# Kernel optimization log

Measured on AMD Instinct MI355X. Metric: run time of the kernel, lower is better.

The kernel has to match this reference:

```python
import jax, jax.numpy as jnp
import numpy as np

B, S, N, E, H = 256, 64, 64, 128, 128
CCLIP = 10.0
NEG = 1e8


def setup_inputs() -> dict:
    key = jax.random.key(0)
    ks = jax.random.split(key, 12)
    u = lambda k, shp, s=1.0: jax.random.uniform(k, shp, minval=-s, maxval=s)
    s = 1.0 / float(np.sqrt(E))
    return dict(
        node_context=jax.random.normal(ks[0], (B, S, N, E), jnp.float32),
        original_data=jax.random.normal(ks[1], (B, S, N, 2), jnp.float32),
        cell_context=jax.random.normal(ks[2], (B, S, E), jnp.float32),
        high_mask=jnp.zeros((B, S), jnp.int32),
        low_mask=jnp.zeros((B, S, N), jnp.int32),
        init_w=u(ks[3], (2 * E,)),
        h_W=u(ks[4], (E, E), s), h_b=jnp.zeros((E,), jnp.float32),
        vw_W=u(ks[5], (2 * E, E), s), vw_b=jnp.zeros((E,), jnp.float32),
        Wq=u(ks[6], (E, H), s), bq=jnp.zeros((H,), jnp.float32),
        Wk=u(ks[7], (E, H), s), bk=jnp.zeros((H,), jnp.float32),
        v=u(ks[8], (H,), s), vb=jnp.zeros((), jnp.float32),
        w_low=u(ks[9], (E,), s),
    )


def _decode(node_context, original_data, cell_context, high_mask, low_mask,
            init_w, h_W, h_b, vw_W, vw_b, Wq, bq, Wk, bk, v, vb, w_low):
    base = jax.random.key(42)
    bidx = jnp.arange(B)
    # query init: h_bar + v_weight_embed(init_w)
    h_bar = cell_context.mean(axis=1) @ h_W + h_b              # [B,E]
    query0 = h_bar + init_w @ vw_W + vw_b                      # [B,E]
    # pointer keys are fixed across steps (target = cell_context)
    keys = jnp.einsum('bse,eh->bsh', cell_context, Wk) + bk    # [B,S,H]

    def step(carry, i):
        query, mask, init_h, last_node = carry
        # Pointer: u = C * tanh(v . tanh(Wq q + Wk t)), masked softmax
        q = query @ Wq + bq                                    # [B,H]
        u_ = jnp.tanh(q[:, None, :] + keys) @ v + vb           # [B,S]
        u_ = CCLIP * jnp.tanh(u_) - NEG * mask.astype(u_.dtype)
        logp = jax.nn.log_softmax(u_, axis=-1)
        idx = jax.random.categorical(jax.random.fold_in(base, i), u_)
        idx = jnp.where(i == 0, jnp.zeros_like(idx), idx)      # forced start cell
        cell_lp = logp[bidx, idx]                              # [B]
        # batched per-cell gathers (replaces the torch per-batch python loop)
        cur_cell = node_context[bidx, idx]                     # [B,N,E]
        orig_cell = original_data[bidx, idx]                   # [B,N,2]
        cur_mask = low_mask[bidx, idx]                         # [B,N]
        # simplified low-level decoder surrogate (external module in torch)
        low_logits = cur_cell @ w_low - NEG * cur_mask.astype(cur_cell.dtype)
        low_lp = jax.nn.log_softmax(low_logits, axis=-1).sum(axis=-1)  # [B]
        low_act = jnp.argmax(low_logits, axis=-1)              # [B]
        i_n = orig_cell[:, 0, :]                               # entry node [B,2]
        l_n = orig_cell[:, -1, :]                              # exit node  [B,2]
        low_reward = jnp.sqrt((jnp.diff(orig_cell, axis=1) ** 2).sum(-1)).sum(-1)
        cell_reward = jnp.sqrt(((last_node - i_n) ** 2).sum(-1))  # [B]
        # Environment.update_state: mask out the visited cell
        mask = jnp.maximum(mask, jax.nn.one_hot(idx, S, dtype=mask.dtype))
        h = cell_context[bidx, idx]                            # [B,E]
        init_h = jnp.where(i == 0, h, init_h)
        query = h_bar + jnp.concatenate([init_h, h], axis=-1) @ vw_W + vw_b
        return (query, mask, init_h, l_n), (cell_lp, low_lp, cell_reward, low_reward, idx, low_act)

    carry0 = (query0, high_mask,
              jnp.zeros((B, E), query0.dtype), jnp.zeros((B, 2), query0.dtype))
    _, (hlp, llp, hr, lr, hact, lact) = jax.lax.scan(step, carry0, jnp.arange(S))
    return (hlp.sum(0), llp.sum(0), hr.sum(0), lr.sum(0), hact.T, lact.T)


def reference(node_context, original_data, cell_context, high_mask, low_mask,
              init_w, h_W, h_b, vw_W, vw_b, Wq, bq, Wk, bk, v, vb, w_low):
    return _decode(node_context, original_data, cell_context, high_mask, low_mask,
                   init_w, h_W, h_b, vw_W, vw_b, Wq, bq, Wk, bk, v, vb, w_low)
```

## Files before the change

### kernel.cpp

```cpp
#include <hip/hip_runtime.h>
#include <stdint.h>


#define NB 256
#define NS 64
#define NN 64
#define NE 128
#define NH 128
#define NEGC 1.0e8f

#define WS_KEYS 0
#define WS_P    (WS_KEYS + NB*NS*NH)
#define WS_C0   (WS_P + NB*NS*NH)
#define WS_Q0   (WS_C0 + NB*NH)
#define WS_U    (WS_Q0 + NB*NH)
#define WS_GUM  (WS_U + NB*65*64)
#define WS_LLP  (WS_GUM + NB*64*64)
#define WS_LRW  (WS_LLP + NB*NS)
#define WS_LAC  (WS_LRW + NB*NS)
#define WS_INX  (WS_LAC + NB*NS)
#define WS_LNX  (WS_INX + NB*NS*2)

__device__ __forceinline__ void tf2x32(uint32_t k0, uint32_t k1,
                                       uint32_t x0, uint32_t x1,
                                       uint32_t &o0, uint32_t &o1) {
  const uint32_t R[5][4] = {{13,15,26,6},{17,29,16,24},{13,15,26,6},{17,29,16,24},{13,15,26,6}};
  uint32_t ks[3] = {k0, k1, k0 ^ k1 ^ 0x1BD11BDAu};
  x0 += ks[0]; x1 += ks[1];
  #pragma unroll
  for (int g = 0; g < 5; ++g) {
    #pragma unroll
    for (int r = 0; r < 4; ++r) {
      x0 += x1;
      uint32_t d = R[g][r];
      x1 = (x1 << d) | (x1 >> (32 - d));
      x1 ^= x0;
    }
    x0 += ks[(g + 1) % 3];
    x1 += ks[(g + 2) % 3] + (uint32_t)(g + 1);
  }
  o0 = x0; o1 = x1;
}

__device__ __forceinline__ float gumbel_from(uint32_t fk0, uint32_t fk1, int e) {
  uint32_t a0, a1, x0, x1;
  if (e < 8192) { x0 = (uint32_t)e; x1 = (uint32_t)(e + 8192); }
  else          { x0 = (uint32_t)(e - 8192); x1 = (uint32_t)e; }
  tf2x32(fk0, fk1, x0, x1, a0, a1);
  uint32_t bits = (e < 8192) ? a0 : a1;
  uint32_t fb = (bits >> 9) | 0x3F800000u;
  float f = __uint_as_float(fb) - 1.0f;
  const float tiny = 1.17549435e-38f;
  float u = fmaxf(tiny, f + tiny);
  return (float)(-log(-log((double)u)));
}

__global__ __launch_bounds__(256) void k_main(
    const float* __restrict__ node,
    const float* __restrict__ orig,
    const float* __restrict__ cellc,
    const int*   __restrict__ lmask,
    const float* __restrict__ init_w,
    const float* __restrict__ hW,
    const float* __restrict__ hb,
    const float* __restrict__ vwW,
    const float* __restrict__ vwb,
    const float* __restrict__ Wq,
    const float* __restrict__ bq,
    const float* __restrict__ Wk,
    const float* __restrict__ bk,
    const float* __restrict__ wlow,
    float* __restrict__ ws)
{
  __shared__ float s_t[NS * 132];
  __shared__ float s_cm[NE], s_hbar[NE], s_base[NE], s_q0e[NE];
  const int t = threadIdx.x;
  const int blk = blockIdx.x;

  if (blk < NB) {
    const int b = blk;
    const float* cb = cellc + (size_t)b * NS * NE;
    const int g = t & 31, sg = t >> 5;
    const int hh0 = 4 * g;

    {
      float acc[8][4];
      #pragma unroll
      for (int r = 0; r < 8; ++r) { acc[r][0]=acc[r][1]=acc[r][2]=acc[r][3]=0.f; }
      for (int k = 0; k < NE; k += 4) {
        float4 w0 = *(const float4*)&Wk[(k+0)*NH+hh0];
        float4 w1 = *(const float4*)&Wk[(k+1)*NH+hh0];
        float4 w2 = *(const float4*)&Wk[(k+2)*NH+hh0];
        float4 w3 = *(const float4*)&Wk[(k+3)*NH+hh0];
        #pragma unroll
        for (int r = 0; r < 8; ++r) {
          float4 c4 = *(const float4*)&cb[(sg*8+r)*NE+k];
          acc[r][0] += c4.x*w0.x + c4.y*w1.x + c4.z*w2.x + c4.w*w3.x;
          acc[r][1] += c4.x*w0.y + c4.y*w1.y + c4.z*w2.y + c4.w*w3.y;
          acc[r][2] += c4.x*w0.z + c4.y*w1.z + c4.z*w2.z + c4.w*w3.z;
          acc[r][3] += c4.x*w0.w + c4.y*w1.w + c4.z*w2.w + c4.w*w3.w;
        }
      }
      float4 bb = *(const float4*)&bk[hh0];
      #pragma unroll
      for (int r = 0; r < 8; ++r) {
        float4 o = make_float4(acc[r][0]+bb.x, acc[r][1]+bb.y, acc[r][2]+bb.z, acc[r][3]+bb.w);
        *(float4*)&ws[WS_KEYS + (size_t)b*NS*NH + (sg*8+r)*NH + hh0] = o;
      }
    }
    {
      const float* Vb = vwW + NE * NE;
      float acc[8][4];
      #pragma unroll
      for (int r = 0; r < 8; ++r) { acc[r][0]=acc[r][1]=acc[r][2]=acc[r][3]=0.f; }
      for (int k = 0; k < NE; k += 4) {
        float4 w0 = *(const float4*)&Vb[(k+0)*NE+hh0];
        float4 w1 = *(const float4*)&Vb[(k+1)*NE+hh0];
        float4 w2 = *(const float4*)&Vb[(k+2)*NE+hh0];
        float4 w3 = *(const float4*)&Vb[(k+3)*NE+hh0];
        #pragma unroll
        for (int r = 0; r < 8; ++r) {
          float4 c4 = *(const float4*)&cb[(sg*8+r)*NE+k];
          acc[r][0] += c4.x*w0.x + c4.y*w1.x + c4.z*w2.x + c4.w*w3.x;
          acc[r][1] += c4.x*w0.y + c4.y*w1.y + c4.z*w2.y + c4.w*w3.y;
          acc[r][2] += c4.x*w0.z + c4.y*w1.z + c4.z*w2.z + c4.w*w3.z;
          acc[r][3] += c4.x*w0.w + c4.y*w1.w + c4.z*w2.w + c4.w*w3.w;
        }
      }
      #pragma unroll
      for (int r = 0; r < 8; ++r)
        *(float4*)&s_t[(sg*8+r)*132 + hh0] =
            make_float4(acc[r][0], acc[r][1], acc[r][2], acc[r][3]);
    }
    if (t < NE) {
      float a = 0.f;
      for (int s = 0; s < NS; ++s) a += cb[s*NE+t];
      s_cm[t] = a * (1.0f/64.0f);
    }
    __syncthreads();
    {
      float acc[8][4];
      #pragma unroll
      for (int r = 0; r < 8; ++r) { acc[r][0]=acc[r][1]=acc[r][2]=acc[r][3]=0.f; }
      for (int k = 0; k < NE; k += 4) {
        float4 w0 = *(const float4*)&Wq[(k+0)*NH+hh0];
        float4 w1 = *(const float4*)&Wq[(k+1)*NH+hh0];
        float4 w2 = *(const float4*)&Wq[(k+2)*NH+hh0];
        float4 w3 = *(const float4*)&Wq[(k+3)*NH+hh0];
        #pragma unroll
        for (int r = 0; r < 8; ++r) {
          float4 c4 = *(const float4*)&s_t[(sg*8+r)*132 + k];
          acc[r][0] += c4.x*w0.x + c4.y*w1.x + c4.z*w2.x + c4.w*w3.x;
          acc[r][1] += c4.x*w0.y + c4.y*w1.y + c4.z*w2.y + c4.w*w3.y;
          acc[r][2] += c4.x*w0.z + c4.y*w1.z + c4.z*w2.z + c4.w*w3.z;
          acc[r][3] += c4.x*w0.w + c4.y*w1.w + c4.z*w2.w + c4.w*w3.w;
        }
      }
      #pragma unroll
      for (int r = 0; r < 8; ++r)
        *(float4*)&ws[WS_P + (size_t)b*NS*NH + (sg*8+r)*NH + hh0] =
            make_float4(acc[r][0], acc[r][1], acc[r][2], acc[r][3]);
    }
    if (t < NE) {
      float a0=0,a1=0,a2=0,a3=0;
      for (int k = 0; k < NE; k += 4) {
        a0 += s_cm[k+0]*hW[(k+0)*NE+t]; a1 += s_cm[k+1]*hW[(k+1)*NE+t];
        a2 += s_cm[k+2]*hW[(k+2)*NE+t]; a3 += s_cm[k+3]*hW[(k+3)*NE+t];
      }
      s_hbar[t] = (a0+a1)+(a2+a3) + hb[t];
    }
    __syncthreads();
    if (t < NE) {
      float a0=0,a1=0,a2=0,a3=0;
      for (int k = 0; k < NE; k += 4) {
        a0 += cb[k+0]*vwW[(k+0)*NE+t]; a1 += cb[k+1]*vwW[(k+1)*NE+t];
        a2 += cb[k+2]*vwW[(k+2)*NE+t]; a3 += cb[k+3]*vwW[(k+3)*NE+t];
      }
      s_base[t] = s_hbar[t] + (a0+a1)+(a2+a3) + vwb[t];
      float e0=0,e1=0,e2=0,e3=0;
      for (int k = 0; k < 2*NE; k += 4) {
        e0 += init_w[k+0]*vwW[(k+0)*NE+t]; e1 += init_w[k+1]*vwW[(k+1)*NE+t];
        e2 += init_w[k+2]*vwW[(k+2)*NE+t]; e3 += init_w[k+3]*vwW[(k+3)*NE+t];
      }
      s_q0e[t] = s_hbar[t] + (e0+e1)+(e2+e3) + vwb[t];
    }
    __syncthreads();
    if (t < NH) {
      float a0=0,a1=0,a2=0,a3=0, b0=0,b1=0,b2=0,b3=0;
      for (int e = 0; e < NE; e += 4) {
        float w0=Wq[(e+0)*NH+t], w1=Wq[(e+1)*NH+t], w2=Wq[(e+2)*NH+t], w3=Wq[(e+3)*NH+t];
        a0 += s_base[e+0]*w0; a1 += s_base[e+1]*w1; a2 += s_base[e+2]*w2; a3 += s_base[e+3]*w3;
        b0 += s_q0e[e+0]*w0;  b1 += s_q0e[e+1]*w1;  b2 += s_q0e[e+2]*w2;  b3 += s_q0e[e+3]*w3;
      }
      ws[WS_C0 + b*NH + t] = (a0+a1)+(a2+a3) + bq[t];
      ws[WS_Q0 + b*NH + t] = (b0+b1)+(b2+b3) + bq[t];
    }
  } else if (blk < NB + 4096) {
    const int l = blk - NB;
    const int b = l >> 4;
    const int w = t >> 6, lane = t & 63;
    const int s = ((l & 15) << 2) + w;
    const size_t row = (size_t)(b*NS + s)*NN + lane;
    const float4* nr4 = (const float4*)(node + row * (size_t)NE);
    const float4* wl4 = (const float4*)wlow;
    float a0=0,a1=0,a2=0,a3=0;
    #pragma unroll 8
    for (int j = 0; j < 32; j += 4) {
      float4 n0=nr4[j], n1=nr4[j+1], n2=nr4[j+2], n3=nr4[j+3];
      float4 w0=wl4[j], w1=wl4[j+1], w2=wl4[j+2], w3=wl4[j+3];
      a0 += n0.x*w0.x + n0.y*w0.y + n0.z*w0.z + n0.w*w0.w;
      a1 += n1.x*w1.x + n1.y*w1.y + n1.z*w1.z + n1.w*w1.w;
      a2 += n2.x*w2.x + n2.y*w2.y + n2.z*w2.z + n2.w*w2.w;
      a3 += n3.x*w3.x + n3.y*w3.y + n3.z*w3.z + n3.w*w3.w;
    }
    float logit = (a0+a1)+(a2+a3) - NEGC * (float)lmask[row];
    float m2 = logit;
    #pragma unroll
    for (int off = 32; off; off >>= 1) m2 = fmaxf(m2, __shfl_xor(m2, off));
    float se = expf(logit - m2);
    float ss = logit;
    float bv = logit; int bi = lane;
    #pragma unroll
    for (int off = 32; off; off >>= 1) {
      se += __shfl_xor(se, off);
      ss += __shfl_xor(ss, off);
      float ov = __shfl_xor(bv, off); int oi = __shfl_xor(bi, off);
      if (ov > bv || (ov == bv && oi < bi)) { bv = ov; bi = oi; }
    }
    float2 og = ((const float2*)orig)[row];
    float nx = __shfl(og.x, (lane+1)&63), ny = __shfl(og.y, (lane+1)&63);
    float dd = 0.f;
    if (lane < 63) {
      float dx = nx - og.x, dy = ny - og.y;
      dd = sqrtf(dx*dx + dy*dy);
    }
    #pragma unroll
    for (int off = 32; off; off >>= 1) dd += __shfl_xor(dd, off);
    const int o = b*NS + s;
    if (lane == 0) {
      ws[WS_LLP + o] = ss - 64.f*(m2 + logf(se));
      ws[WS_LRW + o] = dd;
      ws[WS_LAC + o] = (float)bi;
      ws[WS_INX + 2*o]   = og.x;
      ws[WS_INX + 2*o+1] = og.y;
    }
    if (lane == 63) {
      ws[WS_LNX + 2*o]   = og.x;
      ws[WS_LNX + 2*o+1] = og.y;
    }
  } else {
    const int gblk = blk - NB - 4096;
    const int i = gblk >> 4;
    const int b = ((gblk & 15) << 4) + (t >> 4);
    const int s4 = (t & 15) << 2;
    uint32_t fk0, fk1;
    tf2x32(0u, 42u, 0u, (uint32_t)i, fk0, fk1);
    float4 o;
    o.x = gumbel_from(fk0, fk1, b*64 + s4 + 0);
    o.y = gumbel_from(fk0, fk1, b*64 + s4 + 1);
    o.z = gumbel_from(fk0, fk1, b*64 + s4 + 2);
    o.w = gumbel_from(fk0, fk1, b*64 + s4 + 3);
    *(float4*)&ws[WS_GUM + (size_t)b*4096 + i*64 + s4] = o;
  }
}

__global__ __launch_bounds__(256) void k_u(const float* __restrict__ vvec,
                                           const float* __restrict__ vb_p,
                                           float* __restrict__ ws)
{
  __shared__ float s_keys[NS * 129];
  __shared__ float s_q[4 * NE];
  __shared__ float s_v[NH];
  const int t = threadIdx.x;
  const int b = blockIdx.x >> 3, rb = blockIdx.x & 7;
  const int nrows = (rb == 7) ? 9 : 8;
  {
    const int s = t >> 2, h0 = (t & 3) * 32;
    const float* src = ws + WS_KEYS + (size_t)b*NS*NH + s*NH + h0;
    #pragma unroll
    for (int j = 0; j < 8; ++j) {
      float4 v4 = *(const float4*)&src[4*j];
      s_keys[s*129 + h0 + 4*j + 0] = v4.x;
      s_keys[s*129 + h0 + 4*j + 1] = v4.y;
      s_keys[s*129 + h0 + 4*j + 2] = v4.z;
      s_keys[s*129 + h0 + 4*j + 3] = v4.w;
    }
  }
  if (t < NH) s_v[t] = vvec[t];
  __syncthreads();
  const float vb = vb_p[0];
  const int w = t >> 6, lane = t & 63;
  for (int r = w; r < nrows; r += 4) {
    const int jj = rb*8 + r;
    {
      const float* c0p = ws + WS_C0 + b*NH;
      const float* q0p = ws + WS_Q0 + b*NH;
      const float* Pp  = ws + WS_P + (size_t)b*NS*NH + (size_t)jj*NH;
      float v1, v2;
      if (jj == 64) { v1 = q0p[lane]; v2 = q0p[lane+64]; }
      else          { v1 = c0p[lane] + Pp[lane]; v2 = c0p[lane+64] + Pp[lane+64]; }
      s_q[w*NE + lane]      = v1;
      s_q[w*NE + lane + 64] = v2;
    }
    float acc = 0.f;
    #pragma unroll 4
    for (int h = 0; h < NH; ++h) {
      float qk = s_q[w*NE + h] + s_keys[lane*129 + h];
      acc += tanhf(qk) * s_v[h];
    }
    ws[WS_U + (size_t)b*4160 + jj*64 + lane] = 10.f * tanhf(acc + vb);
  }
}

__global__ __launch_bounds__(64) void k_loop(const int* __restrict__ hmask,
                                             float* __restrict__ out,
                                             const float* __restrict__ ws)
{
  __shared__ float s_U[65 * 64];
  __shared__ float s_gum[64 * 64];
  const int lane = threadIdx.x;
  const int b = blockIdx.x;
  for (int j = lane; j < 65*64; j += 64) s_U[j] = ws[WS_U + (size_t)b*4160 + j];
  for (int j = lane; j < 64*64; j += 64) s_gum[j] = ws[WS_GUM + (size_t)b*4096 + j];
  const int o = b*NS + lane;
  const float lowlp  = ws[WS_LLP + o];
  const float lowrew = ws[WS_LRW + o];
  const float lowact = ws[WS_LAC + o];
  const float inx = ws[WS_INX + 2*o], iny = ws[WS_INX + 2*o+1];
  const float lnx = ws[WS_LNX + 2*o], lny = ws[WS_LNX + 2*o+1];
  float msk = (float)hmask[o];
  float hlp = 0.f, llp = 0.f, hr = 0.f, lr = 0.f;
  float pnx = 0.f, pny = 0.f;
  int prev = 64;
  for (int i = 0; i < NS; ++i) {
    float logit = s_U[prev*64 + lane] - NEGC * msk;
    float pert  = logit + s_gum[i*64 + lane];
    float m = logit, bv = pert; int bi = lane;
    #pragma unroll
    for (int off = 32; off; off >>= 1) {
      m = fmaxf(m, __shfl_xor(m, off));
      float ov = __shfl_xor(bv, off); int oi = __shfl_xor(bi, off);
      if (ov > bv || (ov == bv && oi < bi)) { bv = ov; bi = oi; }
    }
    float se = expf(logit - m);
    #pragma unroll
    for (int off = 32; off; off >>= 1) se += __shfl_xor(se, off);
    const int idx = (i == 0) ? 0 : bi;
    float li = __shfl(logit, idx);
    hlp += li - m - logf(se);
    llp += __shfl(lowlp, idx);
    lr  += __shfl(lowrew, idx);
    float ix = __shfl(inx, idx), iy = __shfl(iny, idx);
    float dx = pnx - ix, dy = pny - iy;
    hr += sqrtf(dx*dx + dy*dy);
    pnx = __shfl(lnx, idx); pny = __shfl(lny, idx);
    float lact_v = __shfl(lowact, idx);
    if (lane == 0) {
      out[4*NB + b*NS + i] = (float)idx;
      out[4*NB + NB*NS + b*NS + i] = lact_v;
    }
    if (lane == idx) msk = 1.f;
    prev = idx;
  }
  if (lane == 0) {
    out[b]        = hlp;
    out[NB + b]   = llp;
    out[2*NB + b] = hr;
    out[3*NB + b] = lr;
  }
}

extern "C" void kernel_launch(void* const* d_in, const int* in_sizes, int n_in,
                              void* d_out, int out_size, void* d_ws, size_t ws_size,
                              hipStream_t stream) {
  (void)in_sizes; (void)n_in; (void)out_size; (void)ws_size;
  const float* node   = (const float*)d_in[0];
  const float* orig   = (const float*)d_in[1];
  const float* cellc  = (const float*)d_in[2];
  const int*   hmask  = (const int*)d_in[3];
  const int*   lmask  = (const int*)d_in[4];
  const float* init_w = (const float*)d_in[5];
  const float* hW     = (const float*)d_in[6];
  const float* hb     = (const float*)d_in[7];
  const float* vwW    = (const float*)d_in[8];
  const float* vwb    = (const float*)d_in[9];
  const float* Wq     = (const float*)d_in[10];
  const float* bq     = (const float*)d_in[11];
  const float* Wk     = (const float*)d_in[12];
  const float* bk     = (const float*)d_in[13];
  const float* v      = (const float*)d_in[14];
  const float* vb     = (const float*)d_in[15];
  const float* wlow   = (const float*)d_in[16];
  float* ws  = (float*)d_ws;
  float* out = (float*)d_out;

  k_main<<<dim3(NB + 4096 + 1024), dim3(256), 0, stream>>>(
      node, orig, cellc, lmask, init_w, hW, hb, vwW, vwb,
      Wq, bq, Wk, bk, wlow, ws);
  k_u<<<dim3(2048), dim3(256), 0, stream>>>(v, vb, ws);
  k_loop<<<dim3(NB), dim3(64), 0, stream>>>(hmask, out, ws);
}
```

Before: 952.0 us.

## Interleave node-context streaming with pointer-logit compute in one fused kernel

The memory-bound low-level node scoring moves out of the prep kernel and into the pointer-logit kernel. Blocks are interleaved in a 2:1 pattern, so bandwidth-heavy streaming overlaps with tanh-heavy compute. The per-batch prep work is split across two blocks to expose more parallelism. Shared-memory key and U/Gumbel staging is vectorized with float4 and a padded stride. The cost is more complex block indexing and one half-block that repeats only part of the prep work.

```diff
diff --git a/kernel.cpp b/kernel.cpp
--- a/kernel.cpp
+++ b/kernel.cpp
@@ -55,11 +55,8 @@
   return (float)(-log(-log((double)u)));
 }
 
-__global__ __launch_bounds__(256) void k_main(
-    const float* __restrict__ node,
-    const float* __restrict__ orig,
+__global__ __launch_bounds__(256) void k_prep(
     const float* __restrict__ cellc,
-    const int*   __restrict__ lmask,
     const float* __restrict__ init_w,
     const float* __restrict__ hW,
     const float* __restrict__ hb,
@@ -69,32 +66,32 @@
     const float* __restrict__ bq,
     const float* __restrict__ Wk,
     const float* __restrict__ bk,
-    const float* __restrict__ wlow,
     float* __restrict__ ws)
 {
-  __shared__ float s_t[NS * 132];
+  __shared__ __align__(16) float s_t[32 * 132];
   __shared__ float s_cm[NE], s_hbar[NE], s_base[NE], s_q0e[NE];
   const int t = threadIdx.x;
   const int blk = blockIdx.x;
 
-  if (blk < NB) {
-    const int b = blk;
+  if (blk < 2 * NB) {
+    const int b = blk >> 1, half = blk & 1, s0 = half * 32;
     const float* cb = cellc + (size_t)b * NS * NE;
     const int g = t & 31, sg = t >> 5;
     const int hh0 = 4 * g;
+    const int r0 = s0 + sg * 4;
 
     {
-      float acc[8][4];
-      #pragma unroll
-      for (int r = 0; r < 8; ++r) { acc[r][0]=acc[r][1]=acc[r][2]=acc[r][3]=0.f; }
+      float acc[4][4];
+      #pragma unroll
+      for (int r = 0; r < 4; ++r) { acc[r][0]=acc[r][1]=acc[r][2]=acc[r][3]=0.f; }
       for (int k = 0; k < NE; k += 4) {
         float4 w0 = *(const float4*)&Wk[(k+0)*NH+hh0];
         float4 w1 = *(const float4*)&Wk[(k+1)*NH+hh0];
         float4 w2 = *(const float4*)&Wk[(k+2)*NH+hh0];
         float4 w3 = *(const float4*)&Wk[(k+3)*NH+hh0];
         #pragma unroll
-        for (int r = 0; r < 8; ++r) {
-          float4 c4 = *(const float4*)&cb[(sg*8+r)*NE+k];
+        for (int r = 0; r < 4; ++r) {
+          float4 c4 = *(const float4*)&cb[(r0+r)*NE+k];
           acc[r][0] += c4.x*w0.x + c4.y*w1.x + c4.z*w2.x + c4.w*w3.x;
           acc[r][1] += c4.x*w0.y + c4.y*w1.y + c4.z*w2.y + c4.w*w3.y;
           acc[r][2] += c4.x*w0.z + c4.y*w1.z + c4.z*w2.z + c4.w*w3.z;
@@ -103,24 +100,23 @@
       }
       float4 bb = *(const float4*)&bk[hh0];
       #pragma unroll
-      for (int r = 0; r < 8; ++r) {
-        float4 o = make_float4(acc[r][0]+bb.x, acc[r][1]+bb.y, acc[r][2]+bb.z, acc[r][3]+bb.w);
-        *(float4*)&ws[WS_KEYS + (size_t)b*NS*NH + (sg*8+r)*NH + hh0] = o;
-      }
+      for (int r = 0; r < 4; ++r)
+        *(float4*)&ws[WS_KEYS + (size_t)b*NS*NH + (r0+r)*NH + hh0] =
+            make_float4(acc[r][0]+bb.x, acc[r][1]+bb.y, acc[r][2]+bb.z, acc[r][3]+bb.w);
     }
     {
       const float* Vb = vwW + NE * NE;
-      float acc[8][4];
-      #pragma unroll
-      for (int r = 0; r < 8; ++r) { acc[r][0]=acc[r][1]=acc[r][2]=acc[r][3]=0.f; }
+      float acc[4][4];
+      #pragma unroll
+      for (int r = 0; r < 4; ++r) { acc[r][0]=acc[r][1]=acc[r][2]=acc[r][3]=0.f; }
       for (int k = 0; k < NE; k += 4) {
         float4 w0 = *(const float4*)&Vb[(k+0)*NE+hh0];
         float4 w1 = *(const float4*)&Vb[(k+1)*NE+hh0];
         float4 w2 = *(const float4*)&Vb[(k+2)*NE+hh0];
         float4 w3 = *(const float4*)&Vb[(k+3)*NE+hh0];
         #pragma unroll
-        for (int r = 0; r < 8; ++r) {
-          float4 c4 = *(const float4*)&cb[(sg*8+r)*NE+k];
+        for (int r = 0; r < 4; ++r) {
+          float4 c4 = *(const float4*)&cb[(r0+r)*NE+k];
           acc[r][0] += c4.x*w0.x + c4.y*w1.x + c4.z*w2.x + c4.w*w3.x;
           acc[r][1] += c4.x*w0.y + c4.y*w1.y + c4.z*w2.y + c4.w*w3.y;
           acc[r][2] += c4.x*w0.z + c4.y*w1.z + c4.z*w2.z + c4.w*w3.z;
@@ -128,28 +124,28 @@
         }
       }
       #pragma unroll
-      for (int r = 0; r < 8; ++r)
-        *(float4*)&s_t[(sg*8+r)*132 + hh0] =
+      for (int r = 0; r < 4; ++r)
+        *(float4*)&s_t[(sg*4+r)*132 + hh0] =
             make_float4(acc[r][0], acc[r][1], acc[r][2], acc[r][3]);
     }
-    if (t < NE) {
+    if (half == 0 && t < NE) {
       float a = 0.f;
       for (int s = 0; s < NS; ++s) a += cb[s*NE+t];
       s_cm[t] = a * (1.0f/64.0f);
     }
     __syncthreads();
     {
-      float acc[8][4];
-      #pragma unroll
-      for (int r = 0; r < 8; ++r) { acc[r][0]=acc[r][1]=acc[r][2]=acc[r][3]=0.f; }
+      float acc[4][4];
+      #pragma unroll
+      for (int r = 0; r < 4; ++r) { acc[r][0]=acc[r][1]=acc[r][2]=acc[r][3]=0.f; }
       for (int k = 0; k < NE; k += 4) {
         float4 w0 = *(const float4*)&Wq[(k+0)*NH+hh0];
         float4 w1 = *(const float4*)&Wq[(k+1)*NH+hh0];
         float4 w2 = *(const float4*)&Wq[(k+2)*NH+hh0];
         float4 w3 = *(const float4*)&Wq[(k+3)*NH+hh0];
         #pragma unroll
-        for (int r = 0; r < 8; ++r) {
-          float4 c4 = *(const float4*)&s_t[(sg*8+r)*132 + k];
+        for (int r = 0; r < 4; ++r) {
+          float4 c4 = *(const float4*)&s_t[(sg*4+r)*132 + k];
           acc[r][0] += c4.x*w0.x + c4.y*w1.x + c4.z*w2.x + c4.w*w3.x;
           acc[r][1] += c4.x*w0.y + c4.y*w1.y + c4.z*w2.y + c4.w*w3.y;
           acc[r][2] += c4.x*w0.z + c4.y*w1.z + c4.z*w2.z + c4.w*w3.z;
@@ -157,99 +153,48 @@
         }
       }
       #pragma unroll
-      for (int r = 0; r < 8; ++r)
-        *(float4*)&ws[WS_P + (size_t)b*NS*NH + (sg*8+r)*NH + hh0] =
+      for (int r = 0; r < 4; ++r)
+        *(float4*)&ws[WS_P + (size_t)b*NS*NH + (r0+r)*NH + hh0] =
             make_float4(acc[r][0], acc[r][1], acc[r][2], acc[r][3]);
     }
-    if (t < NE) {
-      float a0=0,a1=0,a2=0,a3=0;
-      for (int k = 0; k < NE; k += 4) {
-        a0 += s_cm[k+0]*hW[(k+0)*NE+t]; a1 += s_cm[k+1]*hW[(k+1)*NE+t];
-        a2 += s_cm[k+2]*hW[(k+2)*NE+t]; a3 += s_cm[k+3]*hW[(k+3)*NE+t];
-      }
-      s_hbar[t] = (a0+a1)+(a2+a3) + hb[t];
-    }
-    __syncthreads();
-    if (t < NE) {
-      float a0=0,a1=0,a2=0,a3=0;
-      for (int k = 0; k < NE; k += 4) {
-        a0 += cb[k+0]*vwW[(k+0)*NE+t]; a1 += cb[k+1]*vwW[(k+1)*NE+t];
-        a2 += cb[k+2]*vwW[(k+2)*NE+t]; a3 += cb[k+3]*vwW[(k+3)*NE+t];
-      }
-      s_base[t] = s_hbar[t] + (a0+a1)+(a2+a3) + vwb[t];
-      float e0=0,e1=0,e2=0,e3=0;
-      for (int k = 0; k < 2*NE; k += 4) {
-        e0 += init_w[k+0]*vwW[(k+0)*NE+t]; e1 += init_w[k+1]*vwW[(k+1)*NE+t];
-        e2 += init_w[k+2]*vwW[(k+2)*NE+t]; e3 += init_w[k+3]*vwW[(k+3)*NE+t];
-      }
-      s_q0e[t] = s_hbar[t] + (e0+e1)+(e2+e3) + vwb[t];
-    }
-    __syncthreads();
-    if (t < NH) {
-      float a0=0,a1=0,a2=0,a3=0, b0=0,b1=0,b2=0,b3=0;
-      for (int e = 0; e < NE; e += 4) {
-        float w0=Wq[(e+0)*NH+t], w1=Wq[(e+1)*NH+t], w2=Wq[(e+2)*NH+t], w3=Wq[(e+3)*NH+t];
-        a0 += s_base[e+0]*w0; a1 += s_base[e+1]*w1; a2 += s_base[e+2]*w2; a3 += s_base[e+3]*w3;
-        b0 += s_q0e[e+0]*w0;  b1 += s_q0e[e+1]*w1;  b2 += s_q0e[e+2]*w2;  b3 += s_q0e[e+3]*w3;
-      }
-      ws[WS_C0 + b*NH + t] = (a0+a1)+(a2+a3) + bq[t];
-      ws[WS_Q0 + b*NH + t] = (b0+b1)+(b2+b3) + bq[t];
-    }
-  } else if (blk < NB + 4096) {
-    const int l = blk - NB;
-    const int b = l >> 4;
-    const int w = t >> 6, lane = t & 63;
-    const int s = ((l & 15) << 2) + w;
-    const size_t row = (size_t)(b*NS + s)*NN + lane;
-    const float4* nr4 = (const float4*)(node + row * (size_t)NE);
-    const float4* wl4 = (const float4*)wlow;
-    float a0=0,a1=0,a2=0,a3=0;
-    #pragma unroll 8
-    for (int j = 0; j < 32; j += 4) {
-      float4 n0=nr4[j], n1=nr4[j+1], n2=nr4[j+2], n3=nr4[j+3];
-      float4 w0=wl4[j], w1=wl4[j+1], w2=wl4[j+2], w3=wl4[j+3];
-      a0 += n0.x*w0.x + n0.y*w0.y + n0.z*w0.z + n0.w*w0.w;
-      a1 += n1.x*w1.x + n1.y*w1.y + n1.z*w1.z + n1.w*w1.w;
-      a2 += n2.x*w2.x + n2.y*w2.y + n2.z*w2.z + n2.w*w2.w;
-      a3 += n3.x*w3.x + n3.y*w3.y + n3.z*w3.z + n3.w*w3.w;
-    }
-    float logit = (a0+a1)+(a2+a3) - NEGC * (float)lmask[row];
-    float m2 = logit;
-    #pragma unroll
-    for (int off = 32; off; off >>= 1) m2 = fmaxf(m2, __shfl_xor(m2, off));
-    float se = expf(logit - m2);
-    float ss = logit;
-    float bv = logit; int bi = lane;
-    #pragma unroll
-    for (int off = 32; off; off >>= 1) {
-      se += __shfl_xor(se, off);
-      ss += __shfl_xor(ss, off);
-      float ov = __shfl_xor(bv, off); int oi = __shfl_xor(bi, off);
-      if (ov > bv || (ov == bv && oi < bi)) { bv = ov; bi = oi; }
-    }
-    float2 og = ((const float2*)orig)[row];
-    float nx = __shfl(og.x, (lane+1)&63), ny = __shfl(og.y, (lane+1)&63);
-    float dd = 0.f;
-    if (lane < 63) {
-      float dx = nx - og.x, dy = ny - og.y;
-      dd = sqrtf(dx*dx + dy*dy);
-    }
-    #pragma unroll
-    for (int off = 32; off; off >>= 1) dd += __shfl_xor(dd, off);
-    const int o = b*NS + s;
-    if (lane == 0) {
-      ws[WS_LLP + o] = ss - 64.f*(m2 + logf(se));
-      ws[WS_LRW + o] = dd;
-      ws[WS_LAC + o] = (float)bi;
-      ws[WS_INX + 2*o]   = og.x;
-      ws[WS_INX + 2*o+1] = og.y;
-    }
-    if (lane == 63) {
-      ws[WS_LNX + 2*o]   = og.x;
-      ws[WS_LNX + 2*o+1] = og.y;
+    if (half == 0) {
+      if (t < NE) {
+        float a0=0,a1=0,a2=0,a3=0;
+        for (int k = 0; k < NE; k += 4) {
+          a0 += s_cm[k+0]*hW[(k+0)*NE+t]; a1 += s_cm[k+1]*hW[(k+1)*NE+t];
+          a2 += s_cm[k+2]*hW[(k+2)*NE+t]; a3 += s_cm[k+3]*hW[(k+3)*NE+t];
+        }
+        s_hbar[t] = (a0+a1)+(a2+a3) + hb[t];
+      }
+      __syncthreads();
+      if (t < NE) {
+        float a0=0,a1=0,a2=0,a3=0;
+        for (int k = 0; k < NE; k += 4) {
+          a0 += cb[k+0]*vwW[(k+0)*NE+t]; a1 += cb[k+1]*vwW[(k+1)*NE+t];
+          a2 += cb[k+2]*vwW[(k+2)*NE+t]; a3 += cb[k+3]*vwW[(k+3)*NE+t];
+        }
+        s_base[t] = s_hbar[t] + (a0+a1)+(a2+a3) + vwb[t];
+        float e0=0,e1=0,e2=0,e3=0;
+        for (int k = 0; k < 2*NE; k += 4) {
+          e0 += init_w[k+0]*vwW[(k+0)*NE+t]; e1 += init_w[k+1]*vwW[(k+1)*NE+t];
+          e2 += init_w[k+2]*vwW[(k+2)*NE+t]; e3 += init_w[k+3]*vwW[(k+3)*NE+t];
+        }
+        s_q0e[t] = s_hbar[t] + (e0+e1)+(e2+e3) + vwb[t];
+      }
+      __syncthreads();
+      if (t < NH) {
+        float a0=0,a1=0,a2=0,a3=0, b0=0,b1=0,b2=0,b3=0;
+        for (int e = 0; e < NE; e += 4) {
+          float w0=Wq[(e+0)*NH+t], w1=Wq[(e+1)*NH+t], w2=Wq[(e+2)*NH+t], w3=Wq[(e+3)*NH+t];
+          a0 += s_base[e+0]*w0; a1 += s_base[e+1]*w1; a2 += s_base[e+2]*w2; a3 += s_base[e+3]*w3;
+          b0 += s_q0e[e+0]*w0;  b1 += s_q0e[e+1]*w1;  b2 += s_q0e[e+2]*w2;  b3 += s_q0e[e+3]*w3;
+        }
+        ws[WS_C0 + b*NH + t] = (a0+a1)+(a2+a3) + bq[t];
+        ws[WS_Q0 + b*NH + t] = (b0+b1)+(b2+b3) + bq[t];
+      }
     }
   } else {
-    const int gblk = blk - NB - 4096;
+    const int gblk = blk - 2 * NB;
     const int i = gblk >> 4;
     const int b = ((gblk & 15) << 4) + (t >> 4);
     const int s4 = (t & 15) << 2;
@@ -264,51 +209,118 @@
   }
 }
 
-__global__ __launch_bounds__(256) void k_u(const float* __restrict__ vvec,
-                                           const float* __restrict__ vb_p,
-                                           float* __restrict__ ws)
+__global__ __launch_bounds__(256) void k_fused(
+    const float* __restrict__ node,
+    const float* __restrict__ orig,
+    const int*   __restrict__ lmask,
+    const float* __restrict__ vvec,
+    const float* __restrict__ vb_p,
+    const float* __restrict__ wlow,
+    float* __restrict__ ws)
 {
-  __shared__ float s_keys[NS * 129];
-  __shared__ float s_q[4 * NE];
-  __shared__ float s_v[NH];
+  __shared__ __align__(16) float s_keys[NS * 132];
+  __shared__ __align__(16) float s_q[4 * NE];
+  __shared__ __align__(16) float s_v[NH];
   const int t = threadIdx.x;
-  const int b = blockIdx.x >> 3, rb = blockIdx.x & 7;
-  const int nrows = (rb == 7) ? 9 : 8;
-  {
-    const int s = t >> 2, h0 = (t & 3) * 32;
-    const float* src = ws + WS_KEYS + (size_t)b*NS*NH + s*NH + h0;
-    #pragma unroll
-    for (int j = 0; j < 8; ++j) {
-      float4 v4 = *(const float4*)&src[4*j];
-      s_keys[s*129 + h0 + 4*j + 0] = v4.x;
-      s_keys[s*129 + h0 + 4*j + 1] = v4.y;
-      s_keys[s*129 + h0 + 4*j + 2] = v4.z;
-      s_keys[s*129 + h0 + 4*j + 3] = v4.w;
-    }
-  }
-  if (t < NH) s_v[t] = vvec[t];
-  __syncthreads();
-  const float vb = vb_p[0];
+  const int blk = blockIdx.x;
+  const int m3 = blk % 3;
   const int w = t >> 6, lane = t & 63;
-  for (int r = w; r < nrows; r += 4) {
-    const int jj = rb*8 + r;
+
+  if (m3 != 2) {
+    const int u = (blk / 3) * 2 + m3;
+    const int b = u >> 3, rb = u & 7;
+    const int nrows = (rb == 7) ? 9 : 8;
     {
-      const float* c0p = ws + WS_C0 + b*NH;
-      const float* q0p = ws + WS_Q0 + b*NH;
-      const float* Pp  = ws + WS_P + (size_t)b*NS*NH + (size_t)jj*NH;
-      float v1, v2;
-      if (jj == 64) { v1 = q0p[lane]; v2 = q0p[lane+64]; }
-      else          { v1 = c0p[lane] + Pp[lane]; v2 = c0p[lane+64] + Pp[lane+64]; }
-      s_q[w*NE + lane]      = v1;
-      s_q[w*NE + lane + 64] = v2;
-    }
-    float acc = 0.f;
-    #pragma unroll 4
-    for (int h = 0; h < NH; ++h) {
-      float qk = s_q[w*NE + h] + s_keys[lane*129 + h];
-      acc += tanhf(qk) * s_v[h];
-    }
-    ws[WS_U + (size_t)b*4160 + jj*64 + lane] = 10.f * tanhf(acc + vb);
+      const int s = t >> 2, h0 = (t & 3) * 32;
+      const float* src = ws + WS_KEYS + (size_t)b*NS*NH + s*NH + h0;
+      #pragma unroll
+      for (int j = 0; j < 8; ++j)
+        *(float4*)&s_keys[s*132 + h0 + 4*j] = *(const float4*)&src[4*j];
+    }
+    if (t < NH) s_v[t] = vvec[t];
+    __syncthreads();
+    const float vb = vb_p[0];
+    for (int r = w; r < nrows; r += 4) {
+      const int jj = rb*8 + r;
+      {
+        const float* c0p = ws + WS_C0 + b*NH;
+        const float* q0p = ws + WS_Q0 + b*NH;
+        const float* Pp  = ws + WS_P + (size_t)b*NS*NH + (size_t)jj*NH;
+        float v1, v2;
+        if (jj == 64) { v1 = q0p[lane]; v2 = q0p[lane+64]; }
+        else          { v1 = c0p[lane] + Pp[lane]; v2 = c0p[lane+64] + Pp[lane+64]; }
+        s_q[w*NE + lane]      = v1;
+        s_q[w*NE + lane + 64] = v2;
+      }
+      float acc = 0.f;
+      #pragma unroll
+      for (int h = 0; h < NH; h += 4) {
+        float4 k4 = *(const float4*)&s_keys[lane*132 + h];
+        float4 q4 = *(const float4*)&s_q[w*NE + h];
+        float4 v4 = *(const float4*)&s_v[h];
+        acc += tanhf(q4.x + k4.x) * v4.x;
+        acc += tanhf(q4.y + k4.y) * v4.y;
+        acc += tanhf(q4.z + k4.z) * v4.z;
+        acc += tanhf(q4.w + k4.w) * v4.w;
+      }
+      ws[WS_U + (size_t)b*4160 + jj*64 + lane] = 10.f * tanhf(acc + vb);
+    }
+  } else {
+    const int l = blk / 3;
+    const int b = l >> 2;
+    const int sbase = (l & 3) * 16 + w * 4;
+    const float4* wl4 = (const float4*)wlow;
+    #pragma unroll 1
+    for (int r = 0; r < 4; ++r) {
+      const int s = sbase + r;
+      const size_t row = (size_t)(b*NS + s)*NN + lane;
+      const float4* nr4 = (const float4*)(node + row * (size_t)NE);
+      float a0=0,a1=0,a2=0,a3=0;
+      #pragma unroll 4
+      for (int j = 0; j < 32; j += 4) {
+        float4 n0=nr4[j], n1=nr4[j+1], n2=nr4[j+2], n3=nr4[j+3];
+        float4 w0=wl4[j], w1=wl4[j+1], w2=wl4[j+2], w3=wl4[j+3];
+        a0 += n0.x*w0.x + n0.y*w0.y + n0.z*w0.z + n0.w*w0.w;
+        a1 += n1.x*w1.x + n1.y*w1.y + n1.z*w1.z + n1.w*w1.w;
+        a2 += n2.x*w2.x + n2.y*w2.y + n2.z*w2.z + n2.w*w2.w;
+        a3 += n3.x*w3.x + n3.y*w3.y + n3.z*w3.z + n3.w*w3.w;
+      }
+      float logit = (a0+a1)+(a2+a3) - NEGC * (float)lmask[row];
+      float m2 = logit;
+      #pragma unroll
+      for (int off = 32; off; off >>= 1) m2 = fmaxf(m2, __shfl_xor(m2, off));
+      float se = expf(logit - m2);
+      float ss = logit;
+      float bv = logit; int bi = lane;
+      #pragma unroll
+      for (int off = 32; off; off >>= 1) {
+        se += __shfl_xor(se, off);
+        ss += __shfl_xor(ss, off);
+        float ov = __shfl_xor(bv, off); int oi = __shfl_xor(bi, off);
+        if (ov > bv || (ov == bv && oi < bi)) { bv = ov; bi = oi; }
+      }
+      float2 og = ((const float2*)orig)[row];
+      float nx = __shfl(og.x, (lane+1)&63), ny = __shfl(og.y, (lane+1)&63);
+      float dd = 0.f;
+      if (lane < 63) {
+        float dx = nx - og.x, dy = ny - og.y;
+        dd = sqrtf(dx*dx + dy*dy);
+      }
+      #pragma unroll
+      for (int off = 32; off; off >>= 1) dd += __shfl_xor(dd, off);
+      const int o = b*NS + s;
+      if (lane == 0) {
+        ws[WS_LLP + o] = ss - 64.f*(m2 + logf(se));
+        ws[WS_LRW + o] = dd;
+        ws[WS_LAC + o] = (float)bi;
+        ws[WS_INX + 2*o]   = og.x;
+        ws[WS_INX + 2*o+1] = og.y;
+      }
+      if (lane == 63) {
+        ws[WS_LNX + 2*o]   = og.x;
+        ws[WS_LNX + 2*o+1] = og.y;
+      }
+    }
   }
 }
 
@@ -316,12 +328,18 @@
                                              float* __restrict__ out,
                                              const float* __restrict__ ws)
 {
-  __shared__ float s_U[65 * 64];
-  __shared__ float s_gum[64 * 64];
+  __shared__ __align__(16) float s_U[65 * 64];
+  __shared__ __align__(16) float s_gum[64 * 64];
   const int lane = threadIdx.x;
   const int b = blockIdx.x;
-  for (int j = lane; j < 65*64; j += 64) s_U[j] = ws[WS_U + (size_t)b*4160 + j];
-  for (int j = lane; j < 64*64; j += 64) s_gum[j] = ws[WS_GUM + (size_t)b*4096 + j];
+  {
+    const float4* Usrc = (const float4*)(ws + WS_U + (size_t)b*4160);
+    float4* Udst = (float4*)s_U;
+    for (int j = lane; j < 1040; j += 64) Udst[j] = Usrc[j];
+    const float4* Gsrc = (const float4*)(ws + WS_GUM + (size_t)b*4096);
+    float4* Gdst = (float4*)s_gum;
+    for (int j = lane; j < 1024; j += 64) Gdst[j] = Gsrc[j];
+  }
   const int o = b*NS + lane;
   const float lowlp  = ws[WS_LLP + o];
   const float lowrew = ws[WS_LRW + o];
@@ -394,9 +412,9 @@
   float* ws  = (float*)d_ws;
   float* out = (float*)d_out;
 
-  k_main<<<dim3(NB + 4096 + 1024), dim3(256), 0, stream>>>(
-      node, orig, cellc, lmask, init_w, hW, hb, vwW, vwb,
-      Wq, bq, Wk, bk, wlow, ws);
-  k_u<<<dim3(2048), dim3(256), 0, stream>>>(v, vb, ws);
+  k_prep<<<dim3(2*NB + 1024), dim3(256), 0, stream>>>(
+      cellc, init_w, hW, hb, vwW, vwb, Wq, bq, Wk, bk, ws);
+  k_fused<<<dim3(3072), dim3(256), 0, stream>>>(
+      node, orig, lmask, v, vb, wlow, ws);
   k_loop<<<dim3(NB), dim3(64), 0, stream>>>(hmask, out, ws);
 }
```

After: 1.083 ms. 13.7% more time.
